# Performance work log

Hardware: AMD Instinct MI355X
Metric: run time of the kernel (lower is better)

Reference implementation:

```python
import jax, jax.numpy as jnp
import numpy as np

B, L, E, H = 8, 1024, 1024, 16
D = E // H
EPS = 1e-5


def setup_inputs() -> dict:
    key = jax.random.key(0)
    ks = jax.random.split(key, 3)
    s = 1.0 / np.sqrt(E)
    return {
        "x": jax.random.normal(ks[0], (B, L, E), dtype=jnp.float32),
        "w_qkv": jax.random.normal(ks[1], (3 * E, E), dtype=jnp.float32) * s,
        "b_qkv": jnp.zeros((3 * E,), dtype=jnp.float32),
        "w_out": jax.random.normal(ks[2], (E, E), dtype=jnp.float32) * s,
        "b_out": jnp.zeros((E,), dtype=jnp.float32),
        "gamma": jnp.ones((E,), dtype=jnp.float32),
        "beta": jnp.zeros((E,), dtype=jnp.float32),
    }


def reference(x, w_qkv, b_qkv, w_out, b_out, gamma, beta):
    # Packed QKV projection (torch nn.MultiheadAttention in_proj): (B,L,3E)
    qkv = jnp.einsum("ble,fe->blf", x, w_qkv) + b_qkv
    q, k, v = jnp.split(qkv, 3, axis=-1)
    # (B,L,H,D)
    q = q.reshape(B, L, H, D) * (1.0 / np.sqrt(D))
    k = k.reshape(B, L, H, D)
    v = v.reshape(B, L, H, D)
    scores = jnp.einsum("blhd,bmhd->bhlm", q, k)           # (B,H,L,L)
    w = jax.nn.softmax(scores, axis=-1)                     # (B,H,L,L)
    ctx = jnp.einsum("bhlm,bmhd->blhd", w, v).reshape(B, L, E)
    attn_out = jnp.einsum("ble,fe->blf", ctx, w_out) + b_out
    # Residual + LayerNorm
    h = x + attn_out
    mu = h.mean(axis=-1, keepdims=True)
    var = ((h - mu) ** 2).mean(axis=-1, keepdims=True)
    hn = (h - mu) * jax.lax.rsqrt(var + EPS) * gamma + beta
    pooled = hn.mean(axis=1)                                # (B,E)
    # torch returns head-averaged weights (B,L,L); then mean over query dim
    avg_attn = w.mean(axis=1).mean(axis=1)                  # (B,L)
    return pooled, avg_attn
```

## Files before the change

### kernel.cpp

```cpp
#include <hip/hip_runtime.h>
#include <math.h>

constexpr int Bc = 8;
constexpr int Lc = 1024;
constexpr int Ec = 1024;
constexpr int Hc = 16;
constexpr int Dc = 64;
constexpr float EPSc = 1e-5f;

typedef _Float16 f16;
typedef f16 half8 __attribute__((ext_vector_type(8)));
typedef float floatx4 __attribute__((ext_vector_type(4)));

static __device__ inline void gload_lds16(const f16* g, f16* l) {
    __builtin_amdgcn_global_load_lds(
        (const __attribute__((address_space(1))) void*)g,
        (__attribute__((address_space(3))) void*)l, 16, 0, 0);
}

__global__ __launch_bounds__(256)
void cvt_f32_f16_kernel(const float* __restrict__ src, f16* __restrict__ dst, int n8) {
    int i = blockIdx.x * 256 + threadIdx.x;
    const int stride = gridDim.x * 256;
    for (; i < n8; i += stride) {
        float4 a = *(const float4*)(src + (size_t)i * 8);
        float4 b = *(const float4*)(src + (size_t)i * 8 + 4);
        half8 p;
        p[0] = (f16)a.x; p[1] = (f16)a.y; p[2] = (f16)a.z; p[3] = (f16)a.w;
        p[4] = (f16)b.x; p[5] = (f16)b.y; p[6] = (f16)b.z; p[7] = (f16)b.w;
        *(half8*)(dst + (size_t)i * 8) = p;
    }
}

__global__ __launch_bounds__(256)
void gemm_nt_h(const f16* __restrict__ A, const f16* __restrict__ Bm,
               const float* __restrict__ bias, float* __restrict__ Cf,
               f16* __restrict__ Ch, int M, int N, int K) {
    constexpr int TILE = 128;
    constexpr int KT = 64;
    constexpr int RSs = 64;
    __shared__ __align__(16) f16 As[TILE * RSs];
    __shared__ __align__(16) f16 Bs[TILE * RSs];

    const int tid = threadIdx.x;
    const int bm = blockIdx.x * TILE;
    const int bn = blockIdx.y * TILE;

    const int wave = tid >> 6;
    const int lane = tid & 63;
    const int wm = (wave >> 1) * 64;
    const int wn = (wave & 1) * 64;
    const int r16 = lane & 15;
    const int kg = lane >> 4;
    const int kx = r16 & 7;

    floatx4 acc[4][4];
#pragma unroll
    for (int i = 0; i < 4; ++i)
#pragma unroll
        for (int j = 0; j < 4; ++j) acc[i][j] = (floatx4){0.f, 0.f, 0.f, 0.f};

    const int rbase = tid >> 3;
    const int kcg = (tid & 7) ^ (rbase & 7);
    const f16* apt = A + (size_t)(bm + rbase) * K + kcg * 8;
    const f16* bpt = Bm + (size_t)(bn + rbase) * K + kcg * 8;
    f16* asl = As + tid * 8;
    f16* bsl = Bs + tid * 8;

    for (int k0 = 0; k0 < K; k0 += KT) {
        __syncthreads();
#pragma unroll
        for (int q = 0; q < 4; ++q) {
            gload_lds16(apt + (size_t)(q * 32) * K + k0, asl + q * 2048);
            gload_lds16(bpt + (size_t)(q * 32) * K + k0, bsl + q * 2048);
        }
        __syncthreads();

#pragma unroll
        for (int ks = 0; ks < 2; ++ks) {
            const int kslot = ((ks * 4 + kg) ^ kx) * 8;
            half8 af[4], bf[4];
#pragma unroll
            for (int i = 0; i < 4; ++i)
                af[i] = *(const half8*)&As[(wm + 16 * i + r16) * RSs + kslot];
#pragma unroll
            for (int j = 0; j < 4; ++j)
                bf[j] = *(const half8*)&Bs[(wn + 16 * j + r16) * RSs + kslot];
#pragma unroll
            for (int i = 0; i < 4; ++i)
#pragma unroll
                for (int j = 0; j < 4; ++j)
                    acc[i][j] = __builtin_amdgcn_mfma_f32_16x16x32_f16(af[i], bf[j], acc[i][j], 0, 0, 0);
        }
    }

    if (Ch) {
#pragma unroll
        for (int j = 0; j < 4; ++j) {
            const int col = bn + wn + 16 * j + r16;
            const float bv = bias[col];
#pragma unroll
            for (int i = 0; i < 4; ++i) {
                const int row0e = bm + wm + 16 * i + kg * 4;
#pragma unroll
                for (int r = 0; r < 4; ++r)
                    Ch[(size_t)(row0e + r) * N + col] = (f16)(acc[i][j][r] + bv);
            }
        }
    } else {
#pragma unroll
        for (int j = 0; j < 4; ++j) {
            const int col = bn + wn + 16 * j + r16;
            const float bv = bias[col];
#pragma unroll
            for (int i = 0; i < 4; ++i) {
                const int row0e = bm + wm + 16 * i + kg * 4;
#pragma unroll
                for (int r = 0; r < 4; ++r)
                    Cf[(size_t)(row0e + r) * N + col] = acc[i][j][r] + bv;
            }
        }
    }
}

constexpr int AQT = 128;
constexpr int AKT = 128;
constexpr int AKP = 72;
constexpr int AWP = 136;
constexpr int AVP = 136;

constexpr int AQ_OFF  = 0;
constexpr int AKV_OFF = 4608;
constexpr int AW_OFF  = AKV_OFF + 4608;
constexpr int ARS_OFF = AW_OFF + 8704;
constexpr int ACOL_OFF = ARS_OFF + 128;
constexpr int ASMEM   = ACOL_OFF + 1024;

__global__ __launch_bounds__(256, 2)
void attn_kernel(const f16* __restrict__ qkv, f16* __restrict__ ctx,
                 float* __restrict__ avg_out) {
    __shared__ __align__(16) float smemf[ASMEM];
    f16* Kq = (f16*)(smemf + AQ_OFF);
    f16* Kt = (f16*)(smemf + AKV_OFF);
    f16* Vt = (f16*)(smemf + AKV_OFF);
    f16* WS = (f16*)(smemf + AW_OFF);
    float* RS  = smemf + ARS_OFF;
    float* COL = smemf + ACOL_OFF;

    const int tid = threadIdx.x;
    const int qt = blockIdx.x, h = blockIdx.y, b = blockIdx.z;
    const int l0 = qt * AQT;
    const size_t rowstride = 3 * Ec;
    const f16* base = qkv + (size_t)b * Lc * rowstride + (size_t)h * Dc;

    const int wave = tid >> 6, lane = tid & 63;
    const int r16 = lane & 15, kg = lane >> 4;
    const int wm = (wave >> 1) * 64;
    const int wn = (wave & 1) * 64;

    if (tid < 128) RS[tid] = 0.f;
#pragma unroll
    for (int t = 0; t < 4; ++t) COL[t * 256 + tid] = 0.f;

    const int srow = tid >> 1;
    const int sh = (tid & 1) * 32;

    {
        const f16* src = base + (size_t)(l0 + srow) * rowstride + sh;
        f16* dst = Kq + srow * AKP + sh;
#pragma unroll
        for (int jj = 0; jj < 4; ++jj) {
            half8 p = *(const half8*)(src + jj * 8);
#pragma unroll
            for (int e = 0; e < 8; ++e) p[e] = p[e] * (f16)0.125f;
            *(half8*)(dst + jj * 8) = p;
        }
    }

    float rs[4][4];
#pragma unroll
    for (int i = 0; i < 4; ++i)
#pragma unroll
        for (int r = 0; r < 4; ++r) rs[i][r] = 0.f;

    for (int kt = 0; kt < Lc / AKT; ++kt) {
        __syncthreads();
        {
            const f16* src = base + (size_t)(kt * AKT + srow) * rowstride + Ec + sh;
            f16* dst = Kt + srow * AKP + sh;
#pragma unroll
            for (int jj = 0; jj < 4; ++jj)
                *(half8*)(dst + jj * 8) = *(const half8*)(src + jj * 8);
        }
        __syncthreads();

        floatx4 s[4][4];
#pragma unroll
        for (int i = 0; i < 4; ++i)
#pragma unroll
            for (int j = 0; j < 4; ++j) s[i][j] = (floatx4){0.f, 0.f, 0.f, 0.f};
#pragma unroll
        for (int ks = 0; ks < 2; ++ks) {
            half8 af[4], bf[4];
#pragma unroll
            for (int i = 0; i < 4; ++i)
                af[i] = *(const half8*)&Kq[(wm + 16 * i + r16) * AKP + ks * 32 + kg * 8];
#pragma unroll
            for (int j = 0; j < 4; ++j)
                bf[j] = *(const half8*)&Kt[(wn + 16 * j + r16) * AKP + ks * 32 + kg * 8];
#pragma unroll
            for (int i = 0; i < 4; ++i)
#pragma unroll
                for (int j = 0; j < 4; ++j)
                    s[i][j] = __builtin_amdgcn_mfma_f32_16x16x32_f16(af[i], bf[j], s[i][j], 0, 0, 0);
        }
#pragma unroll
        for (int i = 0; i < 4; ++i)
#pragma unroll
            for (int r = 0; r < 4; ++r)
                rs[i][r] += __expf(s[i][0][r]) + __expf(s[i][1][r]) +
                            __expf(s[i][2][r]) + __expf(s[i][3][r]);
    }

#pragma unroll
    for (int i = 0; i < 4; ++i)
#pragma unroll
        for (int r = 0; r < 4; ++r) {
            float v = rs[i][r];
            v += __shfl_xor(v, 1); v += __shfl_xor(v, 2);
            v += __shfl_xor(v, 4); v += __shfl_xor(v, 8);
            rs[i][r] = v;
        }
    if (r16 == 0) {
#pragma unroll
        for (int i = 0; i < 4; ++i)
#pragma unroll
            for (int r = 0; r < 4; ++r)
                atomicAdd(&RS[wm + 16 * i + 4 * kg + r], rs[i][r]);
    }
    __syncthreads();
    if (tid < 128) RS[tid] = 1.0f / RS[tid];
    __syncthreads();

    float rinv[4][4];
#pragma unroll
    for (int i = 0; i < 4; ++i)
#pragma unroll
        for (int r = 0; r < 4; ++r) rinv[i][r] = RS[wm + 16 * i + 4 * kg + r];

    floatx4 cacc[2][4];
#pragma unroll
    for (int p = 0; p < 2; ++p)
#pragma unroll
        for (int j = 0; j < 4; ++j) cacc[p][j] = (floatx4){0.f, 0.f, 0.f, 0.f};
    const int qb = wave * 32;

    for (int kt = 0; kt < Lc / AKT; ++kt) {
        __syncthreads();
        {
            const f16* src = base + (size_t)(kt * AKT + srow) * rowstride + Ec + sh;
            f16* dst = Kt + srow * AKP + sh;
#pragma unroll
            for (int jj = 0; jj < 4; ++jj)
                *(half8*)(dst + jj * 8) = *(const half8*)(src + jj * 8);
        }
        __syncthreads();

        floatx4 s[4][4];
#pragma unroll
        for (int i = 0; i < 4; ++i)
#pragma unroll
            for (int j = 0; j < 4; ++j) s[i][j] = (floatx4){0.f, 0.f, 0.f, 0.f};
#pragma unroll
        for (int ks = 0; ks < 2; ++ks) {
            half8 af[4], bf[4];
#pragma unroll
            for (int i = 0; i < 4; ++i)
                af[i] = *(const half8*)&Kq[(wm + 16 * i + r16) * AKP + ks * 32 + kg * 8];
#pragma unroll
            for (int j = 0; j < 4; ++j)
                bf[j] = *(const half8*)&Kt[(wn + 16 * j + r16) * AKP + ks * 32 + kg * 8];
#pragma unroll
            for (int i = 0; i < 4; ++i)
#pragma unroll
                for (int j = 0; j < 4; ++j)
                    s[i][j] = __builtin_amdgcn_mfma_f32_16x16x32_f16(af[i], bf[j], s[i][j], 0, 0, 0);
        }

        float cs[4] = {0.f, 0.f, 0.f, 0.f};
#pragma unroll
        for (int i = 0; i < 4; ++i)
#pragma unroll
            for (int j = 0; j < 4; ++j)
#pragma unroll
                for (int r = 0; r < 4; ++r) {
                    float w = __expf(s[i][j][r]) * rinv[i][r];
                    s[i][j][r] = w;
                    cs[j] += w;
                }

        __syncthreads();

#pragma unroll
        for (int i = 0; i < 4; ++i)
#pragma unroll
            for (int r = 0; r < 4; ++r) {
                f16* wrow = WS + (wm + 16 * i + 4 * kg + r) * AWP + wn + r16;
#pragma unroll
                for (int j = 0; j < 4; ++j) wrow[16 * j] = (f16)s[i][j][r];
            }

        {
            const f16* src = base + (size_t)(kt * AKT + srow) * rowstride + 2 * Ec + sh;
#pragma unroll
            for (int jj = 0; jj < 4; ++jj) {
                half8 v = *(const half8*)(src + jj * 8);
#pragma unroll
                for (int e = 0; e < 8; ++e)
                    Vt[(sh + jj * 8 + e) * AVP + srow] = v[e];
            }
        }

#pragma unroll
        for (int j = 0; j < 4; ++j) {
            float c = cs[j];
            c += __shfl_xor(c, 16);
            c += __shfl_xor(c, 32);
            if (kg == 0) atomicAdd(&COL[kt * AKT + wn + 16 * j + r16], c);
        }

        __syncthreads();

#pragma unroll
        for (int ks2 = 0; ks2 < 4; ++ks2) {
            half8 wa[2], vb[4];
#pragma unroll
            for (int p = 0; p < 2; ++p)
                wa[p] = *(const half8*)&WS[(qb + 16 * p + r16) * AWP + ks2 * 32 + kg * 8];
#pragma unroll
            for (int j = 0; j < 4; ++j)
                vb[j] = *(const half8*)&Vt[(16 * j + r16) * AVP + ks2 * 32 + kg * 8];
#pragma unroll
            for (int p = 0; p < 2; ++p)
#pragma unroll
                for (int j = 0; j < 4; ++j)
                    cacc[p][j] = __builtin_amdgcn_mfma_f32_16x16x32_f16(wa[p], vb[j], cacc[p][j], 0, 0, 0);
        }
    }

#pragma unroll
    for (int p = 0; p < 2; ++p)
#pragma unroll
        for (int r = 0; r < 4; ++r) {
            f16* dst = ctx + (size_t)(b * Lc + l0 + qb + 16 * p + 4 * kg + r) * Ec + h * Dc + r16;
#pragma unroll
            for (int j = 0; j < 4; ++j) dst[16 * j] = (f16)cacc[p][j][r];
        }

    __syncthreads();
#pragma unroll
    for (int t = 0; t < 4; ++t) {
        int m = t * 256 + tid;
        atomicAdd(&avg_out[b * Lc + m], COL[m] * (1.0f / (Hc * Lc)));
    }
}

__global__ __launch_bounds__(256)
void stats_kernel(const float* __restrict__ x, const float* __restrict__ attn_out,
                  float2* __restrict__ stats) {
    const int row = blockIdx.x;
    const int tid = threadIdx.x;
    const float* xp = x + (size_t)row * Ec;
    const float* ap = attn_out + (size_t)row * Ec;
    float4 xv = *(const float4*)(xp + tid * 4);
    float4 av = *(const float4*)(ap + tid * 4);
    float h0 = xv.x + av.x, h1 = xv.y + av.y, h2 = xv.z + av.z, h3 = xv.w + av.w;
    float s = h0 + h1 + h2 + h3;
    float ss = h0 * h0 + h1 * h1 + h2 * h2 + h3 * h3;
#pragma unroll
    for (int off = 32; off; off >>= 1) {
        s += __shfl_xor(s, off);
        ss += __shfl_xor(ss, off);
    }
    __shared__ float wsum[4], wsq[4];
    const int wave = tid >> 6, lane = tid & 63;
    if (lane == 0) { wsum[wave] = s; wsq[wave] = ss; }
    __syncthreads();
    if (tid == 0) {
        float ts = wsum[0] + wsum[1] + wsum[2] + wsum[3];
        float tq = wsq[0] + wsq[1] + wsq[2] + wsq[3];
        float mean = ts * (1.0f / Ec);
        float var = tq * (1.0f / Ec) - mean * mean;
        stats[row] = make_float2(mean, rsqrtf(var + EPSc));
    }
}

__global__ __launch_bounds__(256)
void pool_kernel(const float* __restrict__ x, const float* __restrict__ attn_out,
                 const float2* __restrict__ stats, const float* __restrict__ gamma,
                 const float* __restrict__ beta, float* __restrict__ pooled) {
    const int b = blockIdx.z;
    const int f = blockIdx.y * 256 + threadIdx.x;
    const int l0 = blockIdx.x * 64;
    const float g = gamma[f];
    const float be = beta[f];
    float acc = 0.f;
    for (int l = l0; l < l0 + 64; ++l) {
        size_t idx = (size_t)(b * Lc + l) * Ec + f;
        float2 st = stats[b * Lc + l];
        float h = x[idx] + attn_out[idx];
        acc += (h - st.x) * st.y * g + be;
    }
    atomicAdd(&pooled[b * Ec + f], acc * (1.0f / Lc));
}

extern "C" void kernel_launch(void* const* d_in, const int* in_sizes, int n_in,
                              void* d_out, int out_size, void* d_ws, size_t ws_size,
                              hipStream_t stream) {
    const float* x      = (const float*)d_in[0];
    const float* w_qkv  = (const float*)d_in[1];
    const float* b_qkv  = (const float*)d_in[2];
    const float* w_out  = (const float*)d_in[3];
    const float* b_out  = (const float*)d_in[4];
    const float* gamma  = (const float*)d_in[5];
    const float* beta   = (const float*)d_in[6];
    float* out = (float*)d_out;

    f16* wsh = (f16*)d_ws;
    f16* qkv_h  = wsh;
    f16* ctx_h  = qkv_h + (size_t)25165824;
    f16* x_h    = ctx_h + (size_t)8388608;
    f16* wqkv_h = x_h + (size_t)8388608;
    f16* wout_h = wqkv_h + (size_t)3145728;
    float* attn_out = (float*)(wout_h + (size_t)1048576);
    float* stats = attn_out + (size_t)8388608;

    const int M = Bc * Lc;

    hipMemsetAsync(d_out, 0, (size_t)out_size * sizeof(float), stream);

    cvt_f32_f16_kernel<<<2048, 256, 0, stream>>>(x, x_h, (Bc * Lc * Ec) / 8);
    cvt_f32_f16_kernel<<<1536, 256, 0, stream>>>(w_qkv, wqkv_h, (3 * Ec * Ec) / 8);
    cvt_f32_f16_kernel<<<512, 256, 0, stream>>>(w_out, wout_h, (Ec * Ec) / 8);

    dim3 g1(M / 128, (3 * Ec) / 128);
    gemm_nt_h<<<g1, 256, 0, stream>>>(x_h, wqkv_h, b_qkv, nullptr, qkv_h, M, 3 * Ec, Ec);

    dim3 g2(Lc / AQT, Hc, Bc);
    attn_kernel<<<g2, 256, 0, stream>>>(qkv_h, ctx_h, out + Bc * Ec);

    dim3 g3(M / 128, Ec / 128);
    gemm_nt_h<<<g3, 256, 0, stream>>>(ctx_h, wout_h, b_out, attn_out, nullptr, M, Ec, Ec);

    stats_kernel<<<M, 256, 0, stream>>>(x, attn_out, (float2*)stats);

    dim3 g5(16, 4, Bc);
    pool_kernel<<<g5, 256, 0, stream>>>(x, attn_out, (float2*)stats, gamma, beta, out);
}
```

Before: 322.1 us.

## Fuse residual into out-proj GEMM, swizzle GEMM tiles, transpose attention score MFMA

```diff
diff --git a/kernel.cpp b/kernel.cpp
--- a/kernel.cpp
+++ b/kernel.cpp
@@ -9,6 +9,7 @@
 constexpr float EPSc = 1e-5f;
 
 typedef _Float16 f16;
+typedef f16 half4 __attribute__((ext_vector_type(4)));
 typedef f16 half8 __attribute__((ext_vector_type(8)));
 typedef float floatx4 __attribute__((ext_vector_type(4)));
 
@@ -34,8 +35,8 @@
 
 __global__ __launch_bounds__(256)
 void gemm_nt_h(const f16* __restrict__ A, const f16* __restrict__ Bm,
-               const float* __restrict__ bias, float* __restrict__ Cf,
-               f16* __restrict__ Ch, int M, int N, int K) {
+               const float* __restrict__ bias, const float* __restrict__ resid,
+               float* __restrict__ Cf, f16* __restrict__ Ch, int M, int N, int K) {
     constexpr int TILE = 128;
     constexpr int KT = 64;
     constexpr int RSs = 64;
@@ -43,8 +44,12 @@
     __shared__ __align__(16) f16 Bs[TILE * RSs];
 
     const int tid = threadIdx.x;
-    const int bm = blockIdx.x * TILE;
-    const int bn = blockIdx.y * TILE;
+    const int nwgx = gridDim.x;
+    const int nwg = nwgx * gridDim.y;
+    const int flat = blockIdx.y * nwgx + blockIdx.x;
+    const int swz = (flat & 7) * (nwg >> 3) + (flat >> 3);
+    const int bm = (swz % nwgx) * TILE;
+    const int bn = (swz / nwgx) * TILE;
 
     const int wave = tid >> 6;
     const int lane = tid & 63;
@@ -116,8 +121,12 @@
             for (int i = 0; i < 4; ++i) {
                 const int row0e = bm + wm + 16 * i + kg * 4;
 #pragma unroll
-                for (int r = 0; r < 4; ++r)
-                    Cf[(size_t)(row0e + r) * N + col] = acc[i][j][r] + bv;
+                for (int r = 0; r < 4; ++r) {
+                    const size_t idx = (size_t)(row0e + r) * N + col;
+                    float v = acc[i][j][r] + bv;
+                    if (resid) v += resid[idx];
+                    Cf[idx] = v;
+                }
             }
         }
     }
@@ -177,11 +186,9 @@
         }
     }
 
-    float rs[4][4];
-#pragma unroll
-    for (int i = 0; i < 4; ++i)
-#pragma unroll
-        for (int r = 0; r < 4; ++r) rs[i][r] = 0.f;
+    float rs[4];
+#pragma unroll
+    for (int i = 0; i < 4; ++i) rs[i] = 0.f;
 
     for (int kt = 0; kt < Lc / AKT; ++kt) {
         __syncthreads();
@@ -196,9 +203,9 @@
 
         floatx4 s[4][4];
 #pragma unroll
-        for (int i = 0; i < 4; ++i)
-#pragma unroll
-            for (int j = 0; j < 4; ++j) s[i][j] = (floatx4){0.f, 0.f, 0.f, 0.f};
+        for (int j = 0; j < 4; ++j)
+#pragma unroll
+            for (int i = 0; i < 4; ++i) s[j][i] = (floatx4){0.f, 0.f, 0.f, 0.f};
 #pragma unroll
         for (int ks = 0; ks < 2; ++ks) {
             half8 af[4], bf[4];
@@ -209,44 +216,41 @@
             for (int j = 0; j < 4; ++j)
                 bf[j] = *(const half8*)&Kt[(wn + 16 * j + r16) * AKP + ks * 32 + kg * 8];
 #pragma unroll
-            for (int i = 0; i < 4; ++i)
-#pragma unroll
-                for (int j = 0; j < 4; ++j)
-                    s[i][j] = __builtin_amdgcn_mfma_f32_16x16x32_f16(af[i], bf[j], s[i][j], 0, 0, 0);
-        }
+            for (int j = 0; j < 4; ++j)
+#pragma unroll
+                for (int i = 0; i < 4; ++i)
+                    s[j][i] = __builtin_amdgcn_mfma_f32_16x16x32_f16(bf[j], af[i], s[j][i], 0, 0, 0);
+        }
+#pragma unroll
+        for (int i = 0; i < 4; ++i) {
+            float t = 0.f;
+#pragma unroll
+            for (int j = 0; j < 4; ++j)
+                t += __expf(s[j][i][0]) + __expf(s[j][i][1]) +
+                     __expf(s[j][i][2]) + __expf(s[j][i][3]);
+            rs[i] += t;
+        }
+    }
+
+#pragma unroll
+    for (int i = 0; i < 4; ++i) {
+        float v = rs[i];
+        v += __shfl_xor(v, 16);
+        v += __shfl_xor(v, 32);
+        rs[i] = v;
+    }
+    if (kg == 0) {
 #pragma unroll
         for (int i = 0; i < 4; ++i)
-#pragma unroll
-            for (int r = 0; r < 4; ++r)
-                rs[i][r] += __expf(s[i][0][r]) + __expf(s[i][1][r]) +
-                            __expf(s[i][2][r]) + __expf(s[i][3][r]);
-    }
-
-#pragma unroll
-    for (int i = 0; i < 4; ++i)
-#pragma unroll
-        for (int r = 0; r < 4; ++r) {
-            float v = rs[i][r];
-            v += __shfl_xor(v, 1); v += __shfl_xor(v, 2);
-            v += __shfl_xor(v, 4); v += __shfl_xor(v, 8);
-            rs[i][r] = v;
-        }
-    if (r16 == 0) {
-#pragma unroll
-        for (int i = 0; i < 4; ++i)
-#pragma unroll
-            for (int r = 0; r < 4; ++r)
-                atomicAdd(&RS[wm + 16 * i + 4 * kg + r], rs[i][r]);
+            atomicAdd(&RS[wm + 16 * i + r16], rs[i]);
     }
     __syncthreads();
     if (tid < 128) RS[tid] = 1.0f / RS[tid];
     __syncthreads();
 
-    float rinv[4][4];
-#pragma unroll
-    for (int i = 0; i < 4; ++i)
-#pragma unroll
-        for (int r = 0; r < 4; ++r) rinv[i][r] = RS[wm + 16 * i + 4 * kg + r];
+    float rinv[4];
+#pragma unroll
+    for (int i = 0; i < 4; ++i) rinv[i] = RS[wm + 16 * i + r16];
 
     floatx4 cacc[2][4];
 #pragma unroll
@@ -268,9 +272,9 @@
 
         floatx4 s[4][4];
 #pragma unroll
-        for (int i = 0; i < 4; ++i)
-#pragma unroll
-            for (int j = 0; j < 4; ++j) s[i][j] = (floatx4){0.f, 0.f, 0.f, 0.f};
+        for (int j = 0; j < 4; ++j)
+#pragma unroll
+            for (int i = 0; i < 4; ++i) s[j][i] = (floatx4){0.f, 0.f, 0.f, 0.f};
 #pragma unroll
         for (int ks = 0; ks < 2; ++ks) {
             half8 af[4], bf[4];
@@ -281,33 +285,38 @@
             for (int j = 0; j < 4; ++j)
                 bf[j] = *(const half8*)&Kt[(wn + 16 * j + r16) * AKP + ks * 32 + kg * 8];
 #pragma unroll
+            for (int j = 0; j < 4; ++j)
+#pragma unroll
+                for (int i = 0; i < 4; ++i)
+                    s[j][i] = __builtin_amdgcn_mfma_f32_16x16x32_f16(bf[j], af[i], s[j][i], 0, 0, 0);
+        }
+
+        float cs[4][4];
+#pragma unroll
+        for (int j = 0; j < 4; ++j)
+#pragma unroll
+            for (int r = 0; r < 4; ++r) cs[j][r] = 0.f;
+#pragma unroll
+        for (int j = 0; j < 4; ++j)
+#pragma unroll
             for (int i = 0; i < 4; ++i)
 #pragma unroll
-                for (int j = 0; j < 4; ++j)
-                    s[i][j] = __builtin_amdgcn_mfma_f32_16x16x32_f16(af[i], bf[j], s[i][j], 0, 0, 0);
-        }
-
-        float cs[4] = {0.f, 0.f, 0.f, 0.f};
-#pragma unroll
-        for (int i = 0; i < 4; ++i)
-#pragma unroll
-            for (int j = 0; j < 4; ++j)
-#pragma unroll
                 for (int r = 0; r < 4; ++r) {
-                    float w = __expf(s[i][j][r]) * rinv[i][r];
-                    s[i][j][r] = w;
-                    cs[j] += w;
+                    float w = __expf(s[j][i][r]) * rinv[i];
+                    s[j][i][r] = w;
+                    cs[j][r] += w;
                 }
 
         __syncthreads();
 
 #pragma unroll
-        for (int i = 0; i < 4; ++i)
-#pragma unroll
-            for (int r = 0; r < 4; ++r) {
-                f16* wrow = WS + (wm + 16 * i + 4 * kg + r) * AWP + wn + r16;
-#pragma unroll
-                for (int j = 0; j < 4; ++j) wrow[16 * j] = (f16)s[i][j][r];
+        for (int j = 0; j < 4; ++j)
+#pragma unroll
+            for (int i = 0; i < 4; ++i) {
+                half4 w4;
+#pragma unroll
+                for (int r = 0; r < 4; ++r) w4[r] = (f16)s[j][i][r];
+                *(half4*)&WS[(wm + 16 * i + r16) * AWP + wn + 16 * j + 4 * kg] = w4;
             }
 
         {
@@ -322,12 +331,14 @@
         }
 
 #pragma unroll
-        for (int j = 0; j < 4; ++j) {
-            float c = cs[j];
-            c += __shfl_xor(c, 16);
-            c += __shfl_xor(c, 32);
-            if (kg == 0) atomicAdd(&COL[kt * AKT + wn + 16 * j + r16], c);
-        }
+        for (int j = 0; j < 4; ++j)
+#pragma unroll
+            for (int r = 0; r < 4; ++r) {
+                float c = cs[j][r];
+                c += __shfl_xor(c, 1); c += __shfl_xor(c, 2);
+                c += __shfl_xor(c, 4); c += __shfl_xor(c, 8);
+                if (r16 == 0) atomicAdd(&COL[kt * AKT + wn + 16 * j + 4 * kg + r], c);
+            }
 
         __syncthreads();
 
@@ -366,17 +377,12 @@
 }
 
 __global__ __launch_bounds__(256)
-void stats_kernel(const float* __restrict__ x, const float* __restrict__ attn_out,
-                  float2* __restrict__ stats) {
+void stats_kernel(const float* __restrict__ hbuf, float2* __restrict__ stats) {
     const int row = blockIdx.x;
     const int tid = threadIdx.x;
-    const float* xp = x + (size_t)row * Ec;
-    const float* ap = attn_out + (size_t)row * Ec;
-    float4 xv = *(const float4*)(xp + tid * 4);
-    float4 av = *(const float4*)(ap + tid * 4);
-    float h0 = xv.x + av.x, h1 = xv.y + av.y, h2 = xv.z + av.z, h3 = xv.w + av.w;
-    float s = h0 + h1 + h2 + h3;
-    float ss = h0 * h0 + h1 * h1 + h2 * h2 + h3 * h3;
+    float4 hv = *(const float4*)(hbuf + (size_t)row * Ec + tid * 4);
+    float s = hv.x + hv.y + hv.z + hv.w;
+    float ss = hv.x * hv.x + hv.y * hv.y + hv.z * hv.z + hv.w * hv.w;
 #pragma unroll
     for (int off = 32; off; off >>= 1) {
         s += __shfl_xor(s, off);
@@ -396,9 +402,9 @@
 }
 
 __global__ __launch_bounds__(256)
-void pool_kernel(const float* __restrict__ x, const float* __restrict__ attn_out,
-                 const float2* __restrict__ stats, const float* __restrict__ gamma,
-                 const float* __restrict__ beta, float* __restrict__ pooled) {
+void pool_kernel(const float* __restrict__ hbuf, const float2* __restrict__ stats,
+                 const float* __restrict__ gamma, const float* __restrict__ beta,
+                 float* __restrict__ pooled) {
     const int b = blockIdx.z;
     const int f = blockIdx.y * 256 + threadIdx.x;
     const int l0 = blockIdx.x * 64;
@@ -408,8 +414,7 @@
     for (int l = l0; l < l0 + 64; ++l) {
         size_t idx = (size_t)(b * Lc + l) * Ec + f;
         float2 st = stats[b * Lc + l];
-        float h = x[idx] + attn_out[idx];
-        acc += (h - st.x) * st.y * g + be;
+        acc += (hbuf[idx] - st.x) * st.y * g + be;
     }
     atomicAdd(&pooled[b * Ec + f], acc * (1.0f / Lc));
 }
@@ -432,8 +437,8 @@
     f16* x_h    = ctx_h + (size_t)8388608;
     f16* wqkv_h = x_h + (size_t)8388608;
     f16* wout_h = wqkv_h + (size_t)3145728;
-    float* attn_out = (float*)(wout_h + (size_t)1048576);
-    float* stats = attn_out + (size_t)8388608;
+    float* hbuf = (float*)(wout_h + (size_t)1048576);
+    float* stats = hbuf + (size_t)8388608;
 
     const int M = Bc * Lc;
 
@@ -444,16 +449,16 @@
     cvt_f32_f16_kernel<<<512, 256, 0, stream>>>(w_out, wout_h, (Ec * Ec) / 8);
 
     dim3 g1(M / 128, (3 * Ec) / 128);
-    gemm_nt_h<<<g1, 256, 0, stream>>>(x_h, wqkv_h, b_qkv, nullptr, qkv_h, M, 3 * Ec, Ec);
+    gemm_nt_h<<<g1, 256, 0, stream>>>(x_h, wqkv_h, b_qkv, nullptr, nullptr, qkv_h, M, 3 * Ec, Ec);
 
     dim3 g2(Lc / AQT, Hc, Bc);
     attn_kernel<<<g2, 256, 0, stream>>>(qkv_h, ctx_h, out + Bc * Ec);
 
     dim3 g3(M / 128, Ec / 128);
-    gemm_nt_h<<<g3, 256, 0, stream>>>(ctx_h, wout_h, b_out, attn_out, nullptr, M, Ec, Ec);
-
-    stats_kernel<<<M, 256, 0, stream>>>(x, attn_out, (float2*)stats);
+    gemm_nt_h<<<g3, 256, 0, stream>>>(ctx_h, wout_h, b_out, x, hbuf, nullptr, M, Ec, Ec);
+
+    stats_kernel<<<M, 256, 0, stream>>>(hbuf, (float2*)stats);
 
     dim3 g5(16, 4, Bc);
-    pool_kernel<<<g5, 256, 0, stream>>>(x, attn_out, (float2*)stats, gamma, beta, out);
-}
+    pool_kernel<<<g5, 256, 0, stream>>>(hbuf, (float2*)stats, gamma, beta, out);
+}
```

After: 362.3 us. 1.12x slower.
